# Optimization experiments

Hardware: AMD Instinct MI355X
Metric: run time of the kernel (lower is better)

The kernel has to match this reference:

```python
import jax, jax.numpy as jnp
import numpy as np

B, S, N, F, H, E = 1, 32, 2048, 64, 128, 32768


def setup_inputs() -> dict:
    key = jax.random.key(0)
    ks = jax.random.split(key, 13)
    p = lambda k, shp: (jax.random.normal(k, shp, dtype=jnp.float32) * 0.05)
    return {
        "x": jax.random.normal(ks[0], (B, S, N, F), dtype=jnp.float32),
        "edge_indexs": jax.random.randint(ks[1], (1, 2, S * E), 0, N, dtype=jnp.int64),
        "edgenum": E,
        "W1": p(ks[2], (F, H)), "b1": p(ks[3], (H,)),
        "W2": p(ks[4], (H, H)), "b2": p(ks[5], (H,)),
        "Wrel": p(ks[6], (H, H)), "brel": p(ks[7], (H,)),
        "Wroot": p(ks[8], (H, H)),
        "W3": p(ks[9], (H, H)), "b3": p(ks[10], (H,)),
        "W4": p(ks[11], (H, 1)), "b4": p(ks[12], (1,)),
    }


def reference(x, edge_indexs, edgenum, W1, b1, W2, b2, Wrel, brel, Wroot, W3, b3, W4, b4):
    batch, seq_len, num_stocks, _ = x.shape
    lrelu = jax.nn.leaky_relu  # default slope 0.01, matches nn.LeakyReLU()
    h = lrelu(x @ W1 + b1)
    h = lrelu(h @ W2 + b2)                       # [B,S,N,H]
    h = h.reshape(seq_len, num_stocks, -1)       # batch==1
    # split of [2, S*E] along edge dim into per-timestep graphs
    edges = edge_indexs[0].reshape(2, seq_len, edgenum)

    def step(h_t, src, tgt):
        # GraphConv(aggr='mean'): lin_rel(mean_j x_j) + lin_root(x_i)
        agg = jax.ops.segment_sum(h_t[src], tgt, num_segments=num_stocks)
        cnt = jax.ops.segment_sum(jnp.ones((edgenum,), h_t.dtype), tgt,
                                  num_segments=num_stocks)
        agg = agg / jnp.maximum(cnt, 1.0)[:, None]
        # all gnn layers share weights and each re-reads output[i], so one
        # application reproduces the original loop's final `out` exactly
        return lrelu(agg @ Wrel + brel + h_t @ Wroot)

    gnn_out = jax.vmap(step)(h, edges[0], edges[1])          # [S,N,H]
    out = gnn_out.reshape(batch, seq_len, num_stocks, -1)
    out = lrelu(out @ W3 + b3)
    out = out @ W4 + b4                                      # [B,S,N,1]
    return out[:, -1].reshape(batch, num_stocks, -1)
```

## Files before the change

### kernel.cpp

```cpp
#include <hip/hip_runtime.h>


#define N_NODES 2048
#define F_IN 64
#define H_DIM 128
#define S_LEN 32
#define E_EDGES 32768
#define T_LAST (S_LEN - 1)
#define CAP 96

__device__ __forceinline__ float lrelu(float v) { return v > 0.0f ? v : 0.01f * v; }

__global__ __launch_bounds__(256) void k_h2(
    const float* __restrict__ x,
    const float* __restrict__ W1, const float* __restrict__ b1,
    const float* __restrict__ W2, const float* __restrict__ b2,
    float* __restrict__ h2, int* __restrict__ deg)
{
    __shared__ float xs[8][F_IN];
    __shared__ float h1s[8][H_DIM];
    const int t = threadIdx.x;
    const int node0 = blockIdx.x * 8;

    if (t < 8) deg[node0 + t] = 0;

    {
        const float* xsrc = x + ((size_t)T_LAST * N_NODES + node0) * F_IN;
        ((float2*)&xs[0][0])[t] = ((const float2*)xsrc)[t];
    }
    __syncthreads();

    const int half = t >> 7;
    const int j = t & 127;
    const int nbase = half * 4;

    {
        float bb = b1[j];
        float acc[4] = {bb, bb, bb, bb};
        for (int k = 0; k < F_IN; ++k) {
            float w = W1[k * H_DIM + j];
            #pragma unroll
            for (int m = 0; m < 4; ++m) acc[m] += xs[nbase + m][k] * w;
        }
        #pragma unroll
        for (int m = 0; m < 4; ++m) h1s[nbase + m][j] = lrelu(acc[m]);
    }
    __syncthreads();

    {
        float bb = b2[j];
        float a2[4] = {bb, bb, bb, bb};
        for (int k = 0; k < H_DIM; ++k) {
            float w = W2[k * H_DIM + j];
            #pragma unroll
            for (int m = 0; m < 4; ++m) a2[m] += h1s[nbase + m][k] * w;
        }
        #pragma unroll
        for (int m = 0; m < 4; ++m)
            h2[(size_t)(node0 + nbase + m) * H_DIM + j] = lrelu(a2[m]);
    }
}

__global__ __launch_bounds__(256) void k_bucket(
    const int* __restrict__ ei, int* __restrict__ deg, int* __restrict__ bucket)
{
    const int e = blockIdx.x * 256 + threadIdx.x;
    const int src = ei[(size_t)T_LAST * E_EDGES + e];
    const int tgt = ei[(size_t)S_LEN * E_EDGES + (size_t)T_LAST * E_EDGES + e];
    const int slot = atomicAdd(&deg[tgt], 1);
    if (slot < CAP) bucket[tgt * CAP + slot] = src;
}

__global__ __launch_bounds__(256) void k_final(
    const float* __restrict__ h2,
    const int* __restrict__ deg, const int* __restrict__ bucket,
    const float* __restrict__ Wrel, const float* __restrict__ brel,
    const float* __restrict__ Wroot,
    const float* __restrict__ W3, const float* __restrict__ b3,
    const float* __restrict__ W4, const float* __restrict__ b4,
    float* __restrict__ out)
{
    __shared__ float aggs[8][H_DIM];
    __shared__ float h2s[8][H_DIM];
    __shared__ float gs[8][H_DIM];
    __shared__ float ps[8][H_DIM];
    __shared__ int   bl[8][CAP];
    __shared__ int   dgs[8];
    const int t = threadIdx.x;
    const int node0 = blockIdx.x * 8;

    ((float4*)&h2s[0][0])[t] = ((const float4*)(h2 + (size_t)node0 * H_DIM))[t];

    {
        const int nidx = t >> 5;
        const int lane = t & 31;
        const int n = node0 + nidx;
        const int dg = min(deg[n], CAP);
        if (lane == 0) dgs[nidx] = dg;
        for (int i = lane; i < dg; i += 32)
            bl[nidx][i] = bucket[n * CAP + i];
    }
    __syncthreads();

    const int half = t >> 7;
    const int j = t & 127;
    const int nbase = half * 4;

    #pragma unroll
    for (int m = 0; m < 4; ++m) {
        const int nidx = nbase + m;
        const int dg = dgs[nidx];
        float acc = 0.0f;
        for (int i = 0; i < dg; ++i) {
            const int src = bl[nidx][i];
            acc += h2[(size_t)src * H_DIM + j];
        }
        aggs[nidx][j] = acc / fmaxf((float)dg, 1.0f);
    }
    __syncthreads();

    {
        float bb = brel[j];
        float acc[4] = {bb, bb, bb, bb};
        for (int k = 0; k < H_DIM; ++k) {
            float wr = Wrel[k * H_DIM + j];
            float wo = Wroot[k * H_DIM + j];
            #pragma unroll
            for (int m = 0; m < 4; ++m)
                acc[m] += aggs[nbase + m][k] * wr + h2s[nbase + m][k] * wo;
        }
        #pragma unroll
        for (int m = 0; m < 4; ++m) gs[nbase + m][j] = lrelu(acc[m]);
    }
    __syncthreads();

    {
        float bb = b3[j];
        float acc[4] = {bb, bb, bb, bb};
        for (int k = 0; k < H_DIM; ++k) {
            float w = W3[k * H_DIM + j];
            #pragma unroll
            for (int m = 0; m < 4; ++m) acc[m] += gs[nbase + m][k] * w;
        }
        const float w4 = W4[j];
        #pragma unroll
        for (int m = 0; m < 4; ++m) ps[nbase + m][j] = lrelu(acc[m]) * w4;
    }
    __syncthreads();

    for (int stride = 64; stride >= 1; stride >>= 1) {
        if (j < stride) {
            #pragma unroll
            for (int m = 0; m < 4; ++m)
                ps[nbase + m][j] += ps[nbase + m][j + stride];
        }
        __syncthreads();
    }
    if (j == 0) {
        const float bb4 = b4[0];
        #pragma unroll
        for (int m = 0; m < 4; ++m)
            out[node0 + nbase + m] = ps[nbase + m][0] + bb4;
    }
}

extern "C" void kernel_launch(void* const* d_in, const int* in_sizes, int n_in,
                              void* d_out, int out_size, void* d_ws, size_t ws_size,
                              hipStream_t stream)
{
    const float* x     = (const float*)d_in[0];
    const int*   ei    = (const int*)d_in[1];
    const float* W1    = (const float*)d_in[3];
    const float* b1    = (const float*)d_in[4];
    const float* W2    = (const float*)d_in[5];
    const float* b2    = (const float*)d_in[6];
    const float* Wrel  = (const float*)d_in[7];
    const float* brel  = (const float*)d_in[8];
    const float* Wroot = (const float*)d_in[9];
    const float* W3    = (const float*)d_in[10];
    const float* b3    = (const float*)d_in[11];
    const float* W4    = (const float*)d_in[12];
    const float* b4    = (const float*)d_in[13];
    float* out = (float*)d_out;

    float* h2     = (float*)d_ws;
    int*   deg    = (int*)(h2 + (size_t)N_NODES * H_DIM);
    int*   bucket = deg + N_NODES;

    k_h2<<<N_NODES / 8, 256, 0, stream>>>(x, W1, b1, W2, b2, h2, deg);
    k_bucket<<<E_EDGES / 256, 256, 0, stream>>>(ei, deg, bucket);
    k_final<<<N_NODES / 8, 256, 0, stream>>>(h2, deg, bucket, Wrel, brel, Wroot,
                                             W3, b3, W4, b4, out);
}
```

Measured before the change: 128.3 us.

## Fuse all three kernels into one persistent kernel with a grid barrier

Merges the MLP, edge bucketing and GNN/head kernels into a single 256-block, 512-thread kernel. A spin-wait grid barrier on a global atomic counter replaces the kernel boundaries, and a memset zeroes the degree and barrier counters. Each thread now handles 2 nodes instead of 4, and the final reduction uses wavefront shuffles instead of a shared-memory tree. This removes launch overhead and inter-kernel gaps. The barrier needs all 256 blocks to be co-resident, otherwise it deadlocks, and it adds a memset call.

```diff
diff --git a/kernel.cpp b/kernel.cpp
--- a/kernel.cpp
+++ b/kernel.cpp
@@ -8,159 +8,139 @@
 #define E_EDGES 32768
 #define T_LAST (S_LEN - 1)
 #define CAP 96
+#define NBLK 256
+#define TPB 512
 
 __device__ __forceinline__ float lrelu(float v) { return v > 0.0f ? v : 0.01f * v; }
 
-__global__ __launch_bounds__(256) void k_h2(
-    const float* __restrict__ x,
+__global__ __launch_bounds__(TPB) void k_fused(
+    const float* __restrict__ x, const int* __restrict__ ei,
     const float* __restrict__ W1, const float* __restrict__ b1,
     const float* __restrict__ W2, const float* __restrict__ b2,
-    float* __restrict__ h2, int* __restrict__ deg)
+    const float* __restrict__ Wrel, const float* __restrict__ brel,
+    const float* __restrict__ Wroot,
+    const float* __restrict__ W3, const float* __restrict__ b3,
+    const float* __restrict__ W4, const float* __restrict__ b4,
+    float* __restrict__ out,
+    int* __restrict__ deg, unsigned int* __restrict__ bar,
+    int* __restrict__ bucket, float* __restrict__ h2)
 {
     __shared__ float xs[8][F_IN];
     __shared__ float h1s[8][H_DIM];
+    __shared__ float aggs[8][H_DIM];
+    __shared__ float h2s[8][H_DIM];
+    __shared__ float gs[8][H_DIM];
+    __shared__ int   bl[8][CAP];
+    __shared__ int   dgs[8];
+    __shared__ float pred[8][2];
+
     const int t = threadIdx.x;
-    const int node0 = blockIdx.x * 8;
+    const int bid = blockIdx.x;
+    const int node0 = bid * 8;
 
-    if (t < 8) deg[node0 + t] = 0;
+    if (t < 128) {
+        const int e = bid * 128 + t;
+        const int src = ei[(size_t)T_LAST * E_EDGES + e];
+        const int tgt = ei[(size_t)(S_LEN + T_LAST) * E_EDGES + e];
+        const int slot = atomicAdd(&deg[tgt], 1);
+        if (slot < CAP) bucket[tgt * CAP + slot] = src;
+    }
 
-    {
+    if (t < 256) {
         const float* xsrc = x + ((size_t)T_LAST * N_NODES + node0) * F_IN;
         ((float2*)&xs[0][0])[t] = ((const float2*)xsrc)[t];
     }
     __syncthreads();
 
-    const int half = t >> 7;
     const int j = t & 127;
-    const int nbase = half * 4;
+    const int q = t >> 7;
+    const int nb = q * 2;
 
     {
-        float bb = b1[j];
-        float acc[4] = {bb, bb, bb, bb};
+        const float bb = b1[j];
+        float a0 = bb, a1 = bb;
         for (int k = 0; k < F_IN; ++k) {
-            float w = W1[k * H_DIM + j];
-            #pragma unroll
-            for (int m = 0; m < 4; ++m) acc[m] += xs[nbase + m][k] * w;
+            const float w = W1[k * H_DIM + j];
+            a0 += xs[nb][k] * w; a1 += xs[nb + 1][k] * w;
         }
-        #pragma unroll
-        for (int m = 0; m < 4; ++m) h1s[nbase + m][j] = lrelu(acc[m]);
+        h1s[nb][j] = lrelu(a0); h1s[nb + 1][j] = lrelu(a1);
+    }
+    __syncthreads();
+    {
+        const float bb = b2[j];
+        float a0 = bb, a1 = bb;
+        for (int k = 0; k < H_DIM; ++k) {
+            const float w = W2[k * H_DIM + j];
+            a0 += h1s[nb][k] * w; a1 += h1s[nb + 1][k] * w;
+        }
+        a0 = lrelu(a0); a1 = lrelu(a1);
+        h2[(size_t)(node0 + nb) * H_DIM + j] = a0;
+        h2[(size_t)(node0 + nb + 1) * H_DIM + j] = a1;
+        h2s[nb][j] = a0; h2s[nb + 1][j] = a1;
+    }
+
+    __syncthreads();
+    if (t == 0) {
+        __hip_atomic_fetch_add(bar, 1u, __ATOMIC_ACQ_REL, __HIP_MEMORY_SCOPE_AGENT);
+        while (__hip_atomic_load(bar, __ATOMIC_ACQUIRE, __HIP_MEMORY_SCOPE_AGENT) < NBLK)
+            __builtin_amdgcn_s_sleep(1);
     }
     __syncthreads();
 
     {
-        float bb = b2[j];
-        float a2[4] = {bb, bb, bb, bb};
-        for (int k = 0; k < H_DIM; ++k) {
-            float w = W2[k * H_DIM + j];
-            #pragma unroll
-            for (int m = 0; m < 4; ++m) a2[m] += h1s[nbase + m][k] * w;
-        }
-        #pragma unroll
-        for (int m = 0; m < 4; ++m)
-            h2[(size_t)(node0 + nbase + m) * H_DIM + j] = lrelu(a2[m]);
-    }
-}
-
-__global__ __launch_bounds__(256) void k_bucket(
-    const int* __restrict__ ei, int* __restrict__ deg, int* __restrict__ bucket)
-{
-    const int e = blockIdx.x * 256 + threadIdx.x;
-    const int src = ei[(size_t)T_LAST * E_EDGES + e];
-    const int tgt = ei[(size_t)S_LEN * E_EDGES + (size_t)T_LAST * E_EDGES + e];
-    const int slot = atomicAdd(&deg[tgt], 1);
-    if (slot < CAP) bucket[tgt * CAP + slot] = src;
-}
-
-__global__ __launch_bounds__(256) void k_final(
-    const float* __restrict__ h2,
-    const int* __restrict__ deg, const int* __restrict__ bucket,
-    const float* __restrict__ Wrel, const float* __restrict__ brel,
-    const float* __restrict__ Wroot,
-    const float* __restrict__ W3, const float* __restrict__ b3,
-    const float* __restrict__ W4, const float* __restrict__ b4,
-    float* __restrict__ out)
-{
-    __shared__ float aggs[8][H_DIM];
-    __shared__ float h2s[8][H_DIM];
-    __shared__ float gs[8][H_DIM];
-    __shared__ float ps[8][H_DIM];
-    __shared__ int   bl[8][CAP];
-    __shared__ int   dgs[8];
-    const int t = threadIdx.x;
-    const int node0 = blockIdx.x * 8;
-
-    ((float4*)&h2s[0][0])[t] = ((const float4*)(h2 + (size_t)node0 * H_DIM))[t];
-
-    {
-        const int nidx = t >> 5;
-        const int lane = t & 31;
-        const int n = node0 + nidx;
+        const int g = t >> 6, lane = t & 63;
+        const int n = node0 + g;
         const int dg = min(deg[n], CAP);
-        if (lane == 0) dgs[nidx] = dg;
-        for (int i = lane; i < dg; i += 32)
-            bl[nidx][i] = bucket[n * CAP + i];
+        if (lane == 0) dgs[g] = dg;
+        for (int i = lane; i < dg; i += 64) bl[g][i] = bucket[n * CAP + i];
     }
     __syncthreads();
 
-    const int half = t >> 7;
-    const int j = t & 127;
-    const int nbase = half * 4;
-
     #pragma unroll
-    for (int m = 0; m < 4; ++m) {
-        const int nidx = nbase + m;
-        const int dg = dgs[nidx];
+    for (int m = 0; m < 2; ++m) {
+        const int n = nb + m;
+        const int dg = dgs[n];
         float acc = 0.0f;
-        for (int i = 0; i < dg; ++i) {
-            const int src = bl[nidx][i];
-            acc += h2[(size_t)src * H_DIM + j];
-        }
-        aggs[nidx][j] = acc / fmaxf((float)dg, 1.0f);
+        for (int i = 0; i < dg; ++i)
+            acc += h2[(size_t)bl[n][i] * H_DIM + j];
+        aggs[n][j] = acc / fmaxf((float)dg, 1.0f);
     }
     __syncthreads();
 
     {
-        float bb = brel[j];
-        float acc[4] = {bb, bb, bb, bb};
+        const float bb = brel[j];
+        float a0 = bb, a1 = bb;
         for (int k = 0; k < H_DIM; ++k) {
-            float wr = Wrel[k * H_DIM + j];
-            float wo = Wroot[k * H_DIM + j];
-            #pragma unroll
-            for (int m = 0; m < 4; ++m)
-                acc[m] += aggs[nbase + m][k] * wr + h2s[nbase + m][k] * wo;
+            const float wr = Wrel[k * H_DIM + j];
+            const float wo = Wroot[k * H_DIM + j];
+            a0 += aggs[nb][k] * wr + h2s[nb][k] * wo;
+            a1 += aggs[nb + 1][k] * wr + h2s[nb + 1][k] * wo;
         }
-        #pragma unroll
-        for (int m = 0; m < 4; ++m) gs[nbase + m][j] = lrelu(acc[m]);
+        gs[nb][j] = lrelu(a0); gs[nb + 1][j] = lrelu(a1);
     }
     __syncthreads();
 
+    float p0, p1;
     {
-        float bb = b3[j];
-        float acc[4] = {bb, bb, bb, bb};
+        const float bb = b3[j];
+        float a0 = bb, a1 = bb;
         for (int k = 0; k < H_DIM; ++k) {
-            float w = W3[k * H_DIM + j];
-            #pragma unroll
-            for (int m = 0; m < 4; ++m) acc[m] += gs[nbase + m][k] * w;
+            const float w = W3[k * H_DIM + j];
+            a0 += gs[nb][k] * w; a1 += gs[nb + 1][k] * w;
         }
         const float w4 = W4[j];
-        #pragma unroll
-        for (int m = 0; m < 4; ++m) ps[nbase + m][j] = lrelu(acc[m]) * w4;
+        p0 = lrelu(a0) * w4; p1 = lrelu(a1) * w4;
     }
+    for (int off = 32; off >= 1; off >>= 1) {
+        p0 += __shfl_down(p0, off);
+        p1 += __shfl_down(p1, off);
+    }
+    const int w = t >> 6;
+    if ((t & 63) == 0) { pred[w][0] = p0; pred[w][1] = p1; }
     __syncthreads();
-
-    for (int stride = 64; stride >= 1; stride >>= 1) {
-        if (j < stride) {
-            #pragma unroll
-            for (int m = 0; m < 4; ++m)
-                ps[nbase + m][j] += ps[nbase + m][j + stride];
-        }
-        __syncthreads();
-    }
-    if (j == 0) {
-        const float bb4 = b4[0];
-        #pragma unroll
-        for (int m = 0; m < 4; ++m)
-            out[node0 + nbase + m] = ps[nbase + m][0] + bb4;
+    if (t < 8) {
+        const int n = t, qq = n >> 1, mm = n & 1;
+        out[node0 + n] = pred[2 * qq][mm] + pred[2 * qq + 1][mm] + b4[0];
     }
 }
 
@@ -183,12 +163,13 @@
     const float* b4    = (const float*)d_in[13];
     float* out = (float*)d_out;
 
-    float* h2     = (float*)d_ws;
-    int*   deg    = (int*)(h2 + (size_t)N_NODES * H_DIM);
-    int*   bucket = deg + N_NODES;
+    int*      deg    = (int*)d_ws;
+    unsigned* bar    = (unsigned*)((int*)d_ws + 2048);
+    int*      bucket = (int*)d_ws + 2064;
+    float*    h2     = (float*)((int*)d_ws + 2064 + N_NODES * CAP);
 
-    k_h2<<<N_NODES / 8, 256, 0, stream>>>(x, W1, b1, W2, b2, h2, deg);
-    k_bucket<<<E_EDGES / 256, 256, 0, stream>>>(ei, deg, bucket);
-    k_final<<<N_NODES / 8, 256, 0, stream>>>(h2, deg, bucket, Wrel, brel, Wroot,
-                                             W3, b3, W4, b4, out);
+    hipMemsetAsync(d_ws, 0, (2048 + 16) * sizeof(int), stream);
+
+    k_fused<<<NBLK, TPB, 0, stream>>>(x, ei, W1, b1, W2, b2, Wrel, brel, Wroot,
+                                      W3, b3, W4, b4, out, deg, bar, bucket, h2);
 }
```

After: 128.1 us. No clear change (-0.2%).
